# Kernel optimization log

Hardware: AMD Instinct MI355X
Metric: run time of the kernel (lower is better)

## Reference

```python
import jax, jax.numpy as jnp
import numpy as np

T, N, E, F, H, OUT = 6, 50000, 800000, 32, 64, 16


def _glorot(key, shape):
    lim = np.sqrt(6.0 / (shape[0] + shape[1])).astype(np.float32)
    return jax.random.uniform(key, shape, jnp.float32, -lim, lim)


def setup_inputs() -> dict:
    key = jax.random.key(0)
    ks = jax.random.split(key, 12)
    return {
        "xs": jax.random.normal(ks[0], (T, N, F), jnp.float32),
        "edge_index": jax.random.randint(ks[1], (T, 2, E), 0, N, jnp.int32),
        # GCNConv weights/biases for the z, r, h gates
        "Wz": _glorot(ks[2], (F, H)), "bz": jnp.zeros((H,), jnp.float32),
        "Wr": _glorot(ks[3], (F, H)), "br": jnp.zeros((H,), jnp.float32),
        "Wh": _glorot(ks[4], (F, H)), "bh": jnp.zeros((H,), jnp.float32),
        # Linear(2H -> H) per gate
        "Lz_W": _glorot(ks[5], (2 * H, H)), "Lz_b": jnp.zeros((H,), jnp.float32),
        "Lr_W": _glorot(ks[6], (2 * H, H)), "Lr_b": jnp.zeros((H,), jnp.float32),
        "Lh_W": _glorot(ks[7], (2 * H, H)), "Lh_b": jnp.zeros((H,), jnp.float32),
        # final Linear(H -> 16)
        "out_W": _glorot(ks[8], (H, OUT)), "out_b": jnp.zeros((OUT,), jnp.float32),
    }


def _gcn(x, W, b, src, dst):
    """GCNConv: D^-1/2 (A+I) D^-1/2 X W + b, edge list form."""
    n = x.shape[0]
    xw = x @ W  # [N,H] project first (cheaper than per-edge)
    loop = jnp.arange(n, dtype=src.dtype)
    s = jnp.concatenate([src, loop])
    d = jnp.concatenate([dst, loop])
    deg = jax.ops.segment_sum(jnp.ones_like(d, jnp.float32), d, num_segments=n)
    dinv = jnp.where(deg > 0, jax.lax.rsqrt(deg), 0.0)
    norm = dinv[s] * dinv[d]          # [E+N]
    msg = xw[s] * norm[:, None]       # gather + scale
    agg = jax.ops.segment_sum(msg, d, num_segments=n)  # scatter-add
    return agg + b


def reference(xs, edge_index, Wz, bz, Wr, br, Wh, bh,
              Lz_W, Lz_b, Lr_W, Lr_b, Lh_W, Lh_b, out_W, out_b):
    n = xs.shape[1]

    def step(h, inp):
        x, src, dst = inp
        Z = jax.nn.sigmoid(jnp.concatenate([_gcn(x, Wz, bz, src, dst), h], -1) @ Lz_W + Lz_b)
        R = jax.nn.sigmoid(jnp.concatenate([_gcn(x, Wr, br, src, dst), h], -1) @ Lr_W + Lr_b)
        Ht = jnp.tanh(jnp.concatenate([_gcn(x, Wh, bh, src, dst), h * R], -1) @ Lh_W + Lh_b)
        h_new = Z * h + (1.0 - Z) * Ht
        return h_new, None

    h0 = jnp.zeros((n, Wz.shape[1]), xs.dtype)
    h_final, _ = jax.lax.scan(step, h0, (xs, edge_index[:, 0], edge_index[:, 1]))
    return h_final @ out_W + out_b  # [N,16]
```

## Files before the change

### kernel.cpp

```cpp
#include <hip/hip_runtime.h>
#include <hip/hip_bf16.h>

#define TT 6
#define NN 50000
#define EE 800000
#define FF 32
#define HH 64
#define OO 16

#define NB 256
#define DPB 196
#define CHUNK 4096
#define CAP 4096

#define WFRAG_N 19456

typedef unsigned short ushort_t;
typedef unsigned char uchar_t;
typedef short short8 __attribute__((ext_vector_type(8)));
typedef float f32x4 __attribute__((ext_vector_type(4)));

__device__ __forceinline__ float ubf(ushort_t v){ return __uint_as_float(((unsigned)v) << 16); }
__device__ __forceinline__ ushort_t f2b(float f){
  unsigned u = __float_as_uint(f);
  return (ushort_t)((u + 0x7FFFu + ((u >> 16) & 1u)) >> 16);
}
__device__ __forceinline__ float lo16f(unsigned u){ return __uint_as_float(u << 16); }
__device__ __forceinline__ float hi16f(unsigned u){ return __uint_as_float(u & 0xFFFF0000u); }

__global__ void prepall_kernel(const float* __restrict__ Wz,const float* __restrict__ bz,
                               const float* __restrict__ Wr,const float* __restrict__ br,
                               const float* __restrict__ Wh,const float* __restrict__ bh,
                               const float* __restrict__ Lz,const float* __restrict__ Lzb,
                               const float* __restrict__ Lr,const float* __restrict__ Lrb,
                               const float* __restrict__ Lh,const float* __restrict__ Lhb,
                               const float* __restrict__ oW,const float* __restrict__ ob,
                               short* __restrict__ wfrag, float* __restrict__ wbias,
                               int* __restrict__ bcur){
  int bid = blockIdx.x, tid = threadIdx.x;
  if (bid < 76){
    int idx = bid*256 + tid;
    int slot = idx >> 9, lane = (idx >> 3) & 63, j = idx & 7;
    int q = lane >> 4, l15 = lane & 15;
    float val;
    if (slot < 36){
      int g, kc, ncol;
      if (slot < 24){ int nt = slot/3; kc = slot - nt*3; ncol = nt*16 + l15;
                      g = (ncol < 64) ? 0 : 1; ncol &= 63; }
      else          { int s2 = slot-24; int nt = s2/3; kc = s2 - nt*3;
                      ncol = nt*16 + l15; g = 2; }
      const float* W = (g==0)?Wz:((g==1)?Wr:Wh);
      const float* L = (g==0)?Lz:((g==1)?Lr:Lh);
      int k = kc*32 + q*8 + j;
      if (k < 32){
        float s = 0.f;
        for (int m = 0; m < 64; m++) s += W[k*64+m] * L[m*64+ncol];
        val = s;
      } else val = L[(32+k)*64 + ncol];
    } else {
      int kc = slot - 36;
      int k = kc*32 + q*8 + j;
      val = oW[k*16 + l15];
    }
    wfrag[idx] = (short)f2b(val);
  } else {
    if (tid < 192){
      int g = tid >> 6, j = tid & 63;
      const float* L  = (g==0)?Lz:((g==1)?Lr:Lh);
      const float* bb = (g==0)?bz:((g==1)?br:bh);
      const float* Lb = (g==0)?Lzb:((g==1)?Lrb:Lhb);
      float s = Lb[j];
      for (int m = 0; m < 64; m++) s += bb[m] * L[m*64+j];
      wbias[tid] = s;
    } else if (tid < 208){
      wbias[tid] = ob[tid-192];
    }
    for (int i = tid; i < 1536; i += 256) bcur[i] = 0;
  }
}

__global__ __launch_bounds__(256) void scatter_kernel(const int* __restrict__ ei,
                                                      int* __restrict__ bcur,
                                                      ushort_t* __restrict__ ssrc16,
                                                      uchar_t* __restrict__ sdst8){
  int t = blockIdx.y;
  __shared__ int cnt[NB];
  __shared__ int lstart[NB];
  __shared__ int gbase[NB];
  __shared__ int wsum[4];
  __shared__ ushort_t spay[CHUNK];
  __shared__ uchar_t  sdlo[CHUNK];
  __shared__ uchar_t  sbk[CHUNK];
  int tid = threadIdx.x;
  cnt[tid] = 0;
  __syncthreads();
  int e0 = blockIdx.x*CHUNK;
  const int* srcs = ei + t*2*EE;
  const int* dsts = ei + t*2*EE + EE;
  int pk[CHUNK/256];
  int ps[CHUNK/256];
  int pd[CHUNK/256];
  #pragma unroll
  for (int i = 0; i < CHUNK/256; i++){
    int e = e0 + i*256 + tid;
    if (e < EE){
      int s = srcs[e], d = dsts[e];
      int b = d / DPB;
      int lr = atomicAdd(&cnt[b], 1);
      pk[i] = (b << 12) | lr;
      ps[i] = s;
      pd[i] = d - b*DPB;
    } else pk[i] = -1;
  }
  __syncthreads();
  {
    int v = cnt[tid];
    int lane = tid & 63, wid = tid >> 6;
    int x = v;
    #pragma unroll
    for (int o = 1; o < 64; o <<= 1){
      int y = __shfl_up(x, o, 64);
      if (lane >= o) x += y;
    }
    if (lane == 63) wsum[wid] = x;
    __syncthreads();
    if (tid == 0){
      int s = 0;
      #pragma unroll
      for (int w = 0; w < 4; w++){ int tmp = wsum[w]; wsum[w] = s; s += tmp; }
    }
    __syncthreads();
    lstart[tid] = x - v + wsum[wid];
    gbase[tid] = (v > 0) ? atomicAdd(&bcur[t*NB + tid], v) : 0;
  }
  __syncthreads();
  #pragma unroll
  for (int i = 0; i < CHUNK/256; i++){
    if (pk[i] >= 0){
      int b = pk[i] >> 12, lr = pk[i] & 4095;
      int pos = lstart[b] + lr;
      spay[pos] = (ushort_t)ps[i];
      sdlo[pos] = (uchar_t)pd[i];
      sbk[pos]  = (uchar_t)b;
    }
  }
  __syncthreads();
  int nE = EE - e0; if (nE > CHUNK) nE = CHUNK;
  for (int i = tid; i < nE; i += 256){
    int b = sbk[i];
    int gpos = gbase[b] + (i - lstart[b]);
    if (gpos < CAP){
      size_t sb = (size_t)(t*NB + b)*CAP + gpos;
      ssrc16[sb] = spay[i];
      sdst8[sb]  = sdlo[i];
    }
  }
}

__global__ __launch_bounds__(256) void degdinv_kernel(const uchar_t* __restrict__ sdst8,
                                                      const int* __restrict__ bcur,
                                                      float* __restrict__ dinv){
  int b = blockIdx.x, t = blockIdx.y, tid = threadIdx.x;
  __shared__ int cnt[DPB];
  for (int i = tid; i < DPB; i += 256) cnt[i] = 0;
  __syncthreads();
  int ecnt = bcur[t*NB + b]; if (ecnt > CAP) ecnt = CAP;
  const uchar_t* dp = sdst8 + (size_t)(t*NB + b)*CAP;
  for (int i = tid; i < ecnt; i += 256)
    atomicAdd(&cnt[dp[i]], 1);
  __syncthreads();
  for (int i = tid; i < DPB; i += 256){
    int n = b*DPB + i;
    if (n < NN) dinv[t*NN + n] = rsqrtf((float)(cnt[i] + 1));
  }
}

__global__ void cvtscale_kernel(const float4* __restrict__ x4,
                                const float* __restrict__ dinv,
                                ushort4* __restrict__ xb4){
  int i = blockIdx.x*256 + threadIdx.x;
  if (i < TT*NN*8){
    float dn = dinv[i >> 3];
    float4 v = x4[i];
    ushort4 o;
    o.x = f2b(v.x*dn); o.y = f2b(v.y*dn); o.z = f2b(v.z*dn); o.w = f2b(v.w*dn);
    xb4[i] = o;
  }
}

__global__ __launch_bounds__(256) void gatherb_kernel(const ushort_t* __restrict__ xbs,
                                                      const ushort_t* __restrict__ ssrc16,
                                                      const uchar_t* __restrict__ sdst8,
                                                      const int* __restrict__ bcur,
                                                      ushort_t* __restrict__ aggb){
  int l = blockIdx.x;
  int wk = ((l & 7) * 192) + (l >> 3);
  int t = wk >> 8;
  int b = wk & 255;
  int tid = threadIdx.x;
  __shared__ ushort_t ssrc[CAP];
  __shared__ uchar_t  sdl[CAP];
  __shared__ int scnt[DPB];
  __shared__ int soff[DPB + 1];
  __shared__ int wsum[4];
  if (tid < DPB) scnt[tid] = 0;
  __syncthreads();
  int ecnt = bcur[t*NB + b]; if (ecnt > CAP) ecnt = CAP;
  size_t slab = (size_t)(t*NB + b)*CAP;
  const ushort_t* sp = ssrc16 + slab;
  const uchar_t*  dp = sdst8 + slab;
  for (int e = tid; e < ecnt; e += 256){
    uchar_t d = dp[e];
    sdl[e] = d;
    atomicAdd(&scnt[d], 1);
  }
  __syncthreads();
  {
    int v = (tid < DPB) ? scnt[tid] : 0;
    int lane = tid & 63, wid = tid >> 6;
    int x = v;
    #pragma unroll
    for (int o = 1; o < 64; o <<= 1){
      int y = __shfl_up(x, o, 64);
      if (lane >= o) x += y;
    }
    if (lane == 63) wsum[wid] = x;
    __syncthreads();
    if (tid == 0){
      int s = 0;
      #pragma unroll
      for (int w = 0; w < 4; w++){ int tmp = wsum[w]; wsum[w] = s; s += tmp; }
    }
    __syncthreads();
    int excl = x - v + wsum[wid];
    if (tid < DPB){ soff[tid] = excl; scnt[tid] = excl; }
    if (tid == DPB-1) soff[DPB] = excl + v;
  }
  __syncthreads();
  for (int e = tid; e < ecnt; e += 256){
    int d = sdl[e];
    int pos = atomicAdd(&scnt[d], 1);
    ssrc[pos] = sp[e];
  }
  __syncthreads();
  int wv = tid >> 6, lane = tid & 63;
  int g = lane >> 3, fp = lane & 7;
  const uint2* xb2 = (const uint2*)xbs + (size_t)t*NN*8;
  uint2* agg2 = (uint2*)aggb + (size_t)t*NN*8;
  for (int bb = wv; bb*8 < DPB; bb += 4){
    int ld = bb*8 + g;
    int e0 = 0, e1 = 0;
    if (ld < DPB){ e0 = soff[ld]; e1 = soff[ld + 1]; }
    float a0 = 0.f, a1 = 0.f, a2 = 0.f, a3 = 0.f;
    for (int i = e0; i < e1; i += 8){
      int sidx[8];
      uint2 rr[8];
      #pragma unroll
      for (int k = 0; k < 8; k++){
        int ik = i + k;
        sidx[k] = (int)ssrc[(ik < e1) ? ik : (e1 - 1)];
      }
      #pragma unroll
      for (int k = 0; k < 8; k++)
        rr[k] = xb2[(size_t)sidx[k]*8 + fp];
      #pragma unroll
      for (int k = 0; k < 8; k++){
        if (i + k >= e1){ rr[k].x = 0u; rr[k].y = 0u; }
        a0 += lo16f(rr[k].x); a1 += hi16f(rr[k].x);
        a2 += lo16f(rr[k].y); a3 += hi16f(rr[k].y);
      }
    }
    int n = b*DPB + ld;
    if (ld < DPB && n < NN){
      float dn = rsqrtf((float)(e1 - e0 + 1));
      uint2 sv = xb2[(size_t)n*8 + fp];
      float o0 = dn*(a0 + lo16f(sv.x));
      float o1 = dn*(a1 + hi16f(sv.x));
      float o2 = dn*(a2 + lo16f(sv.y));
      float o3 = dn*(a3 + hi16f(sv.y));
      uint2 pk;
      pk.x = (unsigned)f2b(o0) | ((unsigned)f2b(o1) << 16);
      pk.y = (unsigned)f2b(o2) | ((unsigned)f2b(o3) << 16);
      agg2[(size_t)n*8 + fp] = pk;
    }
  }
}

__global__ __launch_bounds__(256) void gates_kernel(const ushort_t* __restrict__ aggb,
                                                    const float* __restrict__ wbias,
                                                    const short* __restrict__ wfrag,
                                                    float* __restrict__ out){
  __shared__ __align__(16) short Hsp[4096];
  __shared__ __align__(16) short HRp[4096];
  int tid = threadIdx.x;
  int nb = blockIdx.x*64;
  int wv = tid >> 6, lane = tid & 63;
  int q = lane >> 4, l15 = lane & 15;
  #pragma unroll
  for (int r = 0; r < 8; r++) ((int*)Hsp)[tid + 256*r] = 0;
  short8 wz[3], wr[3], wh[3];
  #pragma unroll
  for (int kc = 0; kc < 3; kc++){
    wz[kc] = ((const short8*)wfrag)[(wv*3 + kc)*64 + lane];
    wr[kc] = ((const short8*)wfrag)[((wv+4)*3 + kc)*64 + lane];
    wh[kc] = ((const short8*)wfrag)[(24 + wv*3 + kc)*64 + lane];
  }
  int jz = wv*16 + l15;
  float cz = wbias[jz], cr = wbias[64 + jz], ch = wbias[128 + jz];
  int c0 = jz >> 3, jl = jz & 7, x0 = c0 & 7;
  int sq0 = q & 7, sq1 = (4 + q) & 7;
  float hreg[4][4];
  #pragma unroll
  for (int mt = 0; mt < 4; mt++)
    #pragma unroll
    for (int e = 0; e < 4; e++) hreg[mt][e] = 0.f;
  f32x4 accZ[4], accH[4];
  const short8* agf = (const short8*)aggb;
  for (int t = 0; t < TT; t++){
    short8 fac[4];
    #pragma unroll
    for (int mt = 0; mt < 4; mt++){
      int gn = nb + mt*16 + l15;
      short8 v = {0,0,0,0,0,0,0,0};
      if (gn < NN) v = agf[((size_t)t*NN + gn)*4 + q];
      fac[mt] = v;
    }
    __syncthreads();
    #pragma unroll
    for (int mt = 0; mt < 4; mt++){
      int n = mt*16 + l15;
      short8 fh0 = *(const short8*)&Hsp[((q)*64   + (n ^ sq0))*8];
      short8 fh1 = *(const short8*)&Hsp[((4+q)*64 + (n ^ sq1))*8];
      f32x4 az = {0.f,0.f,0.f,0.f}, ar = {0.f,0.f,0.f,0.f};
      az = __builtin_amdgcn_mfma_f32_16x16x32_bf16(fac[mt], wz[0], az, 0,0,0);
      az = __builtin_amdgcn_mfma_f32_16x16x32_bf16(fh0,     wz[1], az, 0,0,0);
      az = __builtin_amdgcn_mfma_f32_16x16x32_bf16(fh1,     wz[2], az, 0,0,0);
      ar = __builtin_amdgcn_mfma_f32_16x16x32_bf16(fac[mt], wr[0], ar, 0,0,0);
      ar = __builtin_amdgcn_mfma_f32_16x16x32_bf16(fh0,     wr[1], ar, 0,0,0);
      ar = __builtin_amdgcn_mfma_f32_16x16x32_bf16(fh1,     wr[2], ar, 0,0,0);
      accZ[mt] = az; accH[mt] = ar;
    }
    #pragma unroll
    for (int mt = 0; mt < 4; mt++){
      #pragma unroll
      for (int e = 0; e < 4; e++){
        int node = mt*16 + q*4 + e;
        float z = __builtin_amdgcn_rcpf(1.f + __expf(-(accZ[mt][e] + cz)));
        float r = __builtin_amdgcn_rcpf(1.f + __expf(-(accH[mt][e] + cr)));
        HRp[(c0*64 + (node ^ x0))*8 + jl] = (short)f2b(hreg[mt][e] * r);
        accZ[mt][e] = z;
      }
    }
    __syncthreads();
    #pragma unroll
    for (int mt = 0; mt < 4; mt++){
      int n = mt*16 + l15;
      short8 fr0 = *(const short8*)&HRp[((q)*64   + (n ^ sq0))*8];
      short8 fr1 = *(const short8*)&HRp[((4+q)*64 + (n ^ sq1))*8];
      f32x4 ahh = {0.f,0.f,0.f,0.f};
      ahh = __builtin_amdgcn_mfma_f32_16x16x32_bf16(fac[mt], wh[0], ahh, 0,0,0);
      ahh = __builtin_amdgcn_mfma_f32_16x16x32_bf16(fr0,     wh[1], ahh, 0,0,0);
      ahh = __builtin_amdgcn_mfma_f32_16x16x32_bf16(fr1,     wh[2], ahh, 0,0,0);
      accH[mt] = ahh;
    }
    #pragma unroll
    for (int mt = 0; mt < 4; mt++){
      #pragma unroll
      for (int e = 0; e < 4; e++){
        int node = mt*16 + q*4 + e;
        float xv = accH[mt][e] + ch;
        float ex = __expf(-2.f*fabsf(xv));
        float th = (1.f - ex) * __builtin_amdgcn_rcpf(1.f + ex);
        th = (xv < 0.f) ? -th : th;
        float z = accZ[mt][e];
        float hv = z*hreg[mt][e] + (1.f - z)*th;
        hreg[mt][e] = hv;
        Hsp[(c0*64 + (node ^ x0))*8 + jl] = (short)f2b(hv);
      }
    }
  }
  __syncthreads();
  short8 wo0 = ((const short8*)wfrag)[36*64 + lane];
  short8 wo1 = ((const short8*)wfrag)[37*64 + lane];
  int no = wv*16 + l15;
  short8 f0 = *(const short8*)&Hsp[((q)*64   + (no ^ sq0))*8];
  short8 f1 = *(const short8*)&Hsp[((4+q)*64 + (no ^ sq1))*8];
  f32x4 ao = {0.f,0.f,0.f,0.f};
  ao = __builtin_amdgcn_mfma_f32_16x16x32_bf16(f0, wo0, ao, 0,0,0);
  ao = __builtin_amdgcn_mfma_f32_16x16x32_bf16(f1, wo1, ao, 0,0,0);
  float ob = wbias[192 + l15];
  #pragma unroll
  for (int e = 0; e < 4; e++){
    int gn = nb + wv*16 + q*4 + e;
    if (gn < NN) out[gn*OO + l15] = ao[e] + ob;
  }
}

extern "C" void kernel_launch(void* const* d_in, const int* in_sizes, int n_in,
                              void* d_out, int out_size, void* d_ws, size_t ws_size,
                              hipStream_t stream) {
  const float* xs = (const float*)d_in[0];
  const int*   ei = (const int*)d_in[1];
  float* out = (float*)d_out;
  char* ws = (char*)d_ws;
  ushort_t*  aggb   = (ushort_t*)(ws + 0);
  ushort_t*  xbs    = (ushort_t*)(ws + 19200000);
  ushort_t*  ssrc16 = (ushort_t*)(ws + 38400000);
  uchar_t*   sdst8  = (uchar_t*) (ws + 50982912);
  float*     dinv   = (float*)   (ws + 57274368);
  int*       bcur   = (int*)     (ws + 58474368);
  short*     wfrag  = (short*)   (ws + 58480512);
  float*     wbias  = (float*)   (ws + 58519424);

  prepall_kernel<<<77, 256, 0, stream>>>(
      (const float*)d_in[2],(const float*)d_in[3],(const float*)d_in[4],(const float*)d_in[5],
      (const float*)d_in[6],(const float*)d_in[7],(const float*)d_in[8],(const float*)d_in[9],
      (const float*)d_in[10],(const float*)d_in[11],(const float*)d_in[12],(const float*)d_in[13],
      (const float*)d_in[14],(const float*)d_in[15], wfrag, wbias, bcur);
  scatter_kernel<<<dim3((EE + CHUNK-1)/CHUNK, TT), 256, 0, stream>>>(ei, bcur, ssrc16, sdst8);
  degdinv_kernel<<<dim3(NB, TT), 256, 0, stream>>>(sdst8, bcur, dinv);
  cvtscale_kernel<<<(TT*NN*8 + 255)/256, 256, 0, stream>>>((const float4*)xs, dinv, (ushort4*)xbs);
  gatherb_kernel<<<NB*TT, 256, 0, stream>>>(xbs, ssrc16, sdst8, bcur, aggb);
  gates_kernel<<<(NN + 63)/64, 256, 0, stream>>>(aggb, wbias, wfrag, out);
}
```

Measured before the change: 241.7 us.

## Reuse degree prefix offsets from degdinv in gather and add dynamic destination scheduling

```diff
diff --git a/kernel.cpp b/kernel.cpp
--- a/kernel.cpp
+++ b/kernel.cpp
@@ -27,6 +27,7 @@
 }
 __device__ __forceinline__ float lo16f(unsigned u){ return __uint_as_float(u << 16); }
 __device__ __forceinline__ float hi16f(unsigned u){ return __uint_as_float(u & 0xFFFF0000u); }
+
 
 __global__ void prepall_kernel(const float* __restrict__ Wz,const float* __restrict__ bz,
                                const float* __restrict__ Wr,const float* __restrict__ br,
@@ -159,9 +160,11 @@
 
 __global__ __launch_bounds__(256) void degdinv_kernel(const uchar_t* __restrict__ sdst8,
                                                       const int* __restrict__ bcur,
-                                                      float* __restrict__ dinv){
+                                                      float* __restrict__ dinv,
+                                                      int* __restrict__ soffg){
   int b = blockIdx.x, t = blockIdx.y, tid = threadIdx.x;
   __shared__ int cnt[DPB];
+  __shared__ int wsum[4];
   for (int i = tid; i < DPB; i += 256) cnt[i] = 0;
   __syncthreads();
   int ecnt = bcur[t*NB + b]; if (ecnt > CAP) ecnt = CAP;
@@ -169,6 +172,26 @@
   for (int i = tid; i < ecnt; i += 256)
     atomicAdd(&cnt[dp[i]], 1);
   __syncthreads();
+  int v = (tid < DPB) ? cnt[tid] : 0;
+  {
+    int lane = tid & 63, wid = tid >> 6;
+    int x = v;
+    #pragma unroll
+    for (int o = 1; o < 64; o <<= 1){
+      int y = __shfl_up(x, o, 64);
+      if (lane >= o) x += y;
+    }
+    if (lane == 63) wsum[wid] = x;
+    __syncthreads();
+    if (tid == 0){
+      int s = 0;
+      #pragma unroll
+      for (int w = 0; w < 4; w++){ int tmp = wsum[w]; wsum[w] = s; s += tmp; }
+    }
+    __syncthreads();
+    int excl = x - v + wsum[wid];
+    if (tid <= DPB) soffg[(size_t)(t*NB + b)*(DPB+1) + tid] = excl;
+  }
   for (int i = tid; i < DPB; i += 256){
     int n = b*DPB + i;
     if (n < NN) dinv[t*NN + n] = rsqrtf((float)(cnt[i] + 1));
@@ -192,6 +215,7 @@
                                                       const ushort_t* __restrict__ ssrc16,
                                                       const uchar_t* __restrict__ sdst8,
                                                       const int* __restrict__ bcur,
+                                                      const int* __restrict__ soffg,
                                                       ushort_t* __restrict__ aggb){
   int l = blockIdx.x;
   int wk = ((l & 7) * 192) + (l >> 3);
@@ -199,58 +223,37 @@
   int b = wk & 255;
   int tid = threadIdx.x;
   __shared__ ushort_t ssrc[CAP];
-  __shared__ uchar_t  sdl[CAP];
   __shared__ int scnt[DPB];
   __shared__ int soff[DPB + 1];
-  __shared__ int wsum[4];
-  if (tid < DPB) scnt[tid] = 0;
-  __syncthreads();
+  __shared__ int dcur;
   int ecnt = bcur[t*NB + b]; if (ecnt > CAP) ecnt = CAP;
   size_t slab = (size_t)(t*NB + b)*CAP;
   const ushort_t* sp = ssrc16 + slab;
   const uchar_t*  dp = sdst8 + slab;
+  const int* sg = soffg + (size_t)(t*NB + b)*(DPB+1);
+  if (tid <= DPB){
+    int v = sg[tid];
+    soff[tid] = v;
+    if (tid < DPB) scnt[tid] = v;
+  }
+  if (tid == 0) dcur = 0;
+  __syncthreads();
   for (int e = tid; e < ecnt; e += 256){
-    uchar_t d = dp[e];
-    sdl[e] = d;
-    atomicAdd(&scnt[d], 1);
-  }
-  __syncthreads();
-  {
-    int v = (tid < DPB) ? scnt[tid] : 0;
-    int lane = tid & 63, wid = tid >> 6;
-    int x = v;
-    #pragma unroll
-    for (int o = 1; o < 64; o <<= 1){
-      int y = __shfl_up(x, o, 64);
-      if (lane >= o) x += y;
-    }
-    if (lane == 63) wsum[wid] = x;
-    __syncthreads();
-    if (tid == 0){
-      int s = 0;
-      #pragma unroll
-      for (int w = 0; w < 4; w++){ int tmp = wsum[w]; wsum[w] = s; s += tmp; }
-    }
-    __syncthreads();
-    int excl = x - v + wsum[wid];
-    if (tid < DPB){ soff[tid] = excl; scnt[tid] = excl; }
-    if (tid == DPB-1) soff[DPB] = excl + v;
-  }
-  __syncthreads();
-  for (int e = tid; e < ecnt; e += 256){
-    int d = sdl[e];
+    int d = dp[e];
     int pos = atomicAdd(&scnt[d], 1);
     ssrc[pos] = sp[e];
   }
   __syncthreads();
-  int wv = tid >> 6, lane = tid & 63;
-  int g = lane >> 3, fp = lane & 7;
+  int lane = tid & 63;
+  int fp = lane & 7;
   const uint2* xb2 = (const uint2*)xbs + (size_t)t*NN*8;
   uint2* agg2 = (uint2*)aggb + (size_t)t*NN*8;
-  for (int bb = wv; bb*8 < DPB; bb += 4){
-    int ld = bb*8 + g;
-    int e0 = 0, e1 = 0;
-    if (ld < DPB){ e0 = soff[ld]; e1 = soff[ld + 1]; }
+  while (true){
+    int ld = 0;
+    if ((lane & 7) == 0) ld = atomicAdd(&dcur, 1);
+    ld = __shfl(ld, lane & 56, 64);
+    if (ld >= DPB) break;
+    int e0 = soff[ld], e1 = soff[ld + 1];
     float a0 = 0.f, a1 = 0.f, a2 = 0.f, a3 = 0.f;
     for (int i = e0; i < e1; i += 8){
       int sidx[8];
@@ -271,7 +274,7 @@
       }
     }
     int n = b*DPB + ld;
-    if (ld < DPB && n < NN){
+    if (n < NN){
       float dn = rsqrtf((float)(e1 - e0 + 1));
       uint2 sv = xb2[(size_t)n*8 + fp];
       float o0 = dn*(a0 + lo16f(sv.x));
@@ -411,6 +414,7 @@
   int*       bcur   = (int*)     (ws + 58474368);
   short*     wfrag  = (short*)   (ws + 58480512);
   float*     wbias  = (float*)   (ws + 58519424);
+  int*       soffg  = (int*)     (ws + 58520320);
 
   prepall_kernel<<<77, 256, 0, stream>>>(
       (const float*)d_in[2],(const float*)d_in[3],(const float*)d_in[4],(const float*)d_in[5],
@@ -418,8 +422,8 @@
       (const float*)d_in[10],(const float*)d_in[11],(const float*)d_in[12],(const float*)d_in[13],
       (const float*)d_in[14],(const float*)d_in[15], wfrag, wbias, bcur);
   scatter_kernel<<<dim3((EE + CHUNK-1)/CHUNK, TT), 256, 0, stream>>>(ei, bcur, ssrc16, sdst8);
-  degdinv_kernel<<<dim3(NB, TT), 256, 0, stream>>>(sdst8, bcur, dinv);
+  degdinv_kernel<<<dim3(NB, TT), 256, 0, stream>>>(sdst8, bcur, dinv, soffg);
   cvtscale_kernel<<<(TT*NN*8 + 255)/256, 256, 0, stream>>>((const float4*)xs, dinv, (ushort4*)xbs);
-  gatherb_kernel<<<NB*TT, 256, 0, stream>>>(xbs, ssrc16, sdst8, bcur, aggb);
+  gatherb_kernel<<<NB*TT, 256, 0, stream>>>(xbs, ssrc16, sdst8, bcur, soffg, aggb);
   gates_kernel<<<(NN + 63)/64, 256, 0, stream>>>(aggb, wbias, wfrag, out);
 }
```

New measurement: 239.3 us. No clear change (-1.0%).
